# Performance work log

Measured on AMD Instinct MI355X. Metric: run time of the kernel, lower is better.

Reference implementation:

```python
import jax, jax.numpy as jnp
import numpy as np

KERNEL_SIZE = 25  # moving-average window (matches init kernel_size)


def setup_inputs() -> dict:
    key = jax.random.key(0)
    ks = jax.random.split(key, 5)
    B, T, N, D, O = 128, 336, 325, 3, 96
    return {
        "x": jax.random.normal(ks[0], (B, T, N, D), dtype=jnp.float32),
        "W_season": jax.random.normal(ks[1], (N, T, O), dtype=jnp.float32) * 0.02,
        "b_season": jax.random.normal(ks[2], (N, O), dtype=jnp.float32) * 0.02,
        "W_trend": jax.random.normal(ks[3], (N, T, O), dtype=jnp.float32) * 0.02,
        "b_trend": jax.random.normal(ks[4], (N, O), dtype=jnp.float32) * 0.02,
    }


def _moving_avg(z, k):
    # z: (M, T); replicate-pad (k-1)//2 at both ends, then mean over window k, stride 1.
    p = (k - 1) // 2
    xp = jnp.pad(z, ((0, 0), (p, p)), mode="edge")
    cs = jnp.concatenate(
        [jnp.zeros((z.shape[0], 1), z.dtype), jnp.cumsum(xp, axis=1)], axis=1
    )
    return (cs[:, k:] - cs[:, :-k]) / k  # (M, T) for odd k


def reference(x, W_season, b_season, W_trend, b_trend):
    B, T, N, D = x.shape
    O = W_season.shape[-1]
    # (B,T,N,D) -> (B,N,D,T) -> flat (B*N*D, T)
    z = x.transpose(0, 2, 3, 1).reshape(B * N * D, T)
    mean = _moving_avg(z, KERNEL_SIZE)
    res = z - mean
    BD = B * D
    # Faithful to the original slicing res[B*n*D : B*(n+1)*D]: contiguous blocks
    # of B*D rows per node -> reshape to (N, B*D, T).
    res_n = res.reshape(N, BD, T)
    mean_n = mean.reshape(N, BD, T)
    out_res = jnp.einsum("nbt,nto->nbo", res_n, W_season) + b_season[:, None, :]
    out_mean = jnp.einsum("nbt,nto->nbo", mean_n, W_trend) + b_trend[:, None, :]
    out = (out_res + out_mean).transpose(1, 0, 2)  # stack dim=1 -> (B*D, N, O)
    # torch .view(B, N, D, O) on contiguous (B*D, N, O), then permute(0,3,1,2)
    out = out.reshape(B, N, D, O).transpose(0, 3, 1, 2)  # (B, O, N, D)
    return out
```

## Files before the change

kernel.cpp:

```cpp
#include <hip/hip_runtime.h>
#include <hip/hip_bf16.h>

typedef __attribute__((ext_vector_type(8))) short short8;
typedef __attribute__((ext_vector_type(4))) float f32x4;
typedef unsigned short ushort_t;
typedef unsigned int uint32;

#define T_DIM   336
#define N_NODES 325
#define O_DIM   96
#define BD      384
#define ND      975
#define XB      327600
#define KT      96
#define NSTEP   4
#define MT      128
#define AST     104
#define BST     104
#define BSEG    10240
#define WTO     32256
#define WP_T    120

static __device__ __forceinline__ uint32 pk2bf(float a, float b) {
    union { __hip_bfloat16 h; ushort_t u; } x, y;
    x.h = __float2bfloat16(a); y.h = __float2bfloat16(b);
    return ((uint32)y.u << 16) | x.u;
}

static __device__ __forceinline__ void gload_lds16(const void* g, void* l) {
    __builtin_amdgcn_global_load_lds(
        (const __attribute__((address_space(1))) void*)g,
        (__attribute__((address_space(3))) void*)l, 16, 0, 0);
}

__global__ __launch_bounds__(576)
void dlinear_wprep(const float* __restrict__ Ws, const float* __restrict__ bs,
                   const float* __restrict__ Wt, const float* __restrict__ bt,
                   ushort_t* __restrict__ Bpack, float* __restrict__ biasArr)
{
    __shared__ float Wdl[WP_T][O_DIM];
    const int nn  = blockIdx.x;
    const int s   = blockIdx.y;
    const int tid = threadIdx.x;
    const int t0  = s * KT;

    const float* wsn = Ws + (size_t)nn * WTO;
    const float* wtn = Wt + (size_t)nn * WTO;

    #pragma unroll
    for (int it = 0; it < 20; ++it) {
        int i = tid + it*576;
        int t = i / O_DIM;
        int o = i - t*O_DIM;
        int tg = t0 - 12 + t;
        float v = 0.f;
        if (tg >= 0 && tg < T_DIM) v = wtn[tg*O_DIM + o] - wsn[tg*O_DIM + o];
        Wdl[t][o] = v;
    }
    if (s == 0 && tid < O_DIM)
        biasArr[nn*O_DIM + tid] = bs[nn*O_DIM + tid] + bt[nn*O_DIM + tid];
    __syncthreads();

    const int kc = tid / O_DIM;
    const int o  = tid - kc*O_DIM;
    const int k0 = kc * 16;

    float S = 0.f;
    #pragma unroll
    for (int j = 0; j < 25; ++j) S += Wdl[k0 + j][o];

    uint32* bp32 = (uint32*)(Bpack + (size_t)(nn*4 + s) * BSEG + o * BST);
    float prev = 0.f;
    #pragma unroll
    for (int j = 0; j < 16; ++j) {
        const int k = k0 + j;
        const int v = t0 + k;
        float val = 0.f;
        if (v < T_DIM) {
            float V = S;
            if (v == 0) {
                V = 0.f;
                #pragma unroll
                for (int t = 0; t <= 12; ++t) V += (float)(13 - t) * Wdl[12 + t][o];
            } else if (v == T_DIM - 1) {
                V = 0.f;
                #pragma unroll
                for (int t = 0; t <= 12; ++t) V += (float)(t + 1) * Wdl[47 + t][o];
            }
            val = wsn[v*O_DIM + o] + V * (1.0f/25.0f);
        }
        if (j & 1) bp32[k >> 1] = pk2bf(prev, val); else prev = val;
        if (j < 15) S += Wdl[k + 25][o] - Wdl[k][o];
    }
    if (kc == 0) {
        bp32[48] = 0u; bp32[49] = 0u; bp32[50] = 0u; bp32[51] = 0u;
    }
}

__global__ __launch_bounds__(512, 6)
void dlinear_gemm(const float* __restrict__ x,
                  const ushort_t* __restrict__ Bpack,
                  const float* __restrict__ biasArr,
                  float* __restrict__ Cws)
{
    __shared__ ushort_t Btile[BSEG];
    __shared__ ushort_t Atile[MT][AST];

    const int tid = threadIdx.x;
    const int bid = blockIdx.x;
    const int nn  = bid / 3;
    const int m0  = (bid % 3) * MT;
    const int r_base = nn * BD + m0;

    const int m   = tid & (MT-1);
    const int tb  = (tid >> 7) * 24;
    const int r   = r_base + m;
    const int bI  = r / ND;
    const int rem = r - bI * ND;
    const float* xp = x + (size_t)bI * XB + rem;

    const ushort_t* bsrc = Bpack + (size_t)nn * (4*BSEG);

    const int wave = tid >> 6;
    const int lane = tid & 63;
    const int wm = wave & 3;
    const int wn = wave >> 2;
    const int a_row0 = wm*32 + (lane & 15);
    const int b_col0 = wn*48 + (lane & 15);
    const int ksub   = (lane >> 4) * 8;

    f32x4 acc[2][3];
    #pragma unroll
    for (int i = 0; i < 2; ++i)
        #pragma unroll
        for (int j = 0; j < 3; ++j)
            acc[i][j] = (f32x4){0.f, 0.f, 0.f, 0.f};

    for (int s = 0; s < NSTEP; ++s) {
        __syncthreads();

        {
            const ushort_t* bs_s = bsrc + (size_t)s * BSEG;
            gload_lds16(bs_s + (size_t)tid*8,        &Btile[tid*8]);
            gload_lds16(bs_s + (size_t)(tid+512)*8,  &Btile[(tid+512)*8]);
            if (tid < 256)
                gload_lds16(bs_s + (size_t)(tid+1024)*8, &Btile[(tid+1024)*8]);
        }

        const int t0 = s * KT;
        #pragma unroll
        for (int h = 0; h < 2; ++h) {
            float v[12];
            #pragma unroll
            for (int u = 0; u < 12; ++u) {
                int t  = t0 + tb + h*12 + u;
                int tc = t < T_DIM ? t : (T_DIM-1);
                v[u] = __builtin_nontemporal_load(&xp[tc * ND]);
            }
            uint32 p[6];
            #pragma unroll
            for (int u = 0; u < 6; ++u) p[u] = pk2bf(v[2*u], v[2*u+1]);
            uint32* arow = (uint32*)&Atile[m][tb + h*12];
            *(uint2*)&arow[0] = make_uint2(p[0], p[1]);
            *(uint2*)&arow[2] = make_uint2(p[2], p[3]);
            *(uint2*)&arow[4] = make_uint2(p[4], p[5]);
        }
        __syncthreads();

        #pragma unroll
        for (int kc = 0; kc < 3; ++kc) {
            const int k = kc*32 + ksub;
            short8 a0 = *(const short8*)&Atile[a_row0     ][k];
            short8 a1 = *(const short8*)&Atile[a_row0 + 16][k];
            short8 b0 = *(const short8*)&Btile[(b_col0     )*BST + k];
            short8 b1 = *(const short8*)&Btile[(b_col0 + 16)*BST + k];
            short8 b2 = *(const short8*)&Btile[(b_col0 + 32)*BST + k];
            acc[0][0] = __builtin_amdgcn_mfma_f32_16x16x32_bf16(a0, b0, acc[0][0], 0, 0, 0);
            acc[1][0] = __builtin_amdgcn_mfma_f32_16x16x32_bf16(a1, b0, acc[1][0], 0, 0, 0);
            acc[0][1] = __builtin_amdgcn_mfma_f32_16x16x32_bf16(a0, b1, acc[0][1], 0, 0, 0);
            acc[1][1] = __builtin_amdgcn_mfma_f32_16x16x32_bf16(a1, b1, acc[1][1], 0, 0, 0);
            acc[0][2] = __builtin_amdgcn_mfma_f32_16x16x32_bf16(a0, b2, acc[0][2], 0, 0, 0);
            acc[1][2] = __builtin_amdgcn_mfma_f32_16x16x32_bf16(a1, b2, acc[1][2], 0, 0, 0);
        }
    }

    float* Cbase = Cws + (size_t)r_base * O_DIM;
    const float* bfp = biasArr + nn * O_DIM;
    const int rsub = (lane >> 4) * 4;
    #pragma unroll
    for (int fm = 0; fm < 2; ++fm) {
        #pragma unroll
        for (int fn = 0; fn < 3; ++fn) {
            const int col = b_col0 + fn*16;
            const float bv = bfp[col];
            #pragma unroll
            for (int j = 0; j < 4; ++j) {
                const int rowm = wm*32 + fm*16 + rsub + j;
                Cbase[rowm*O_DIM + col] = acc[fm][fn][j] + bv;
            }
        }
    }
}

__global__ __launch_bounds__(256)
void dlinear_out(const float* __restrict__ Cws, float* __restrict__ out)
{
    __shared__ float tile[65][97];
    const int m   = blockIdx.x;
    const int nn0 = blockIdx.y * 65;
    const int tid = threadIdx.x;

    for (int idx = tid; idx < 65*O_DIM; idx += 256) {
        int nni = idx / O_DIM;
        int o   = idx - nni*O_DIM;
        tile[nni][o] = Cws[(size_t)((nn0 + nni)*BD + m)*O_DIM + o];
    }
    __syncthreads();
    const int b = m / 3;
    const int g = m - b*3;
    float* obase = out + (size_t)b*93600 + g*N_NODES + nn0;
    for (int idx = tid; idx < 65*O_DIM; idx += 256) {
        int o   = idx / 65;
        int nni = idx - o*65;
        obase[o*ND + nni] = tile[nni][o];
    }
}

extern "C" void kernel_launch(void* const* d_in, const int* in_sizes, int n_in,
                              void* d_out, int out_size, void* d_ws, size_t ws_size,
                              hipStream_t stream)
{
    const float* x  = (const float*)d_in[0];
    const float* Ws = (const float*)d_in[1];
    const float* bs = (const float*)d_in[2];
    const float* Wt = (const float*)d_in[3];
    const float* bt = (const float*)d_in[4];
    float* out = (float*)d_out;
    float* Cws = (float*)d_ws;

    ushort_t* Bpack  = (ushort_t*)d_out;
    float*    biasAr = (float*)d_out + 6656000;

    dlinear_wprep<<<dim3(N_NODES, 4), dim3(576), 0, stream>>>(Ws, bs, Wt, bt, Bpack, biasAr);
    dlinear_gemm <<<dim3(975),        dim3(512), 0, stream>>>(x, Bpack, biasAr, Cws);
    dlinear_out  <<<dim3(384, 5),     dim3(256), 0, stream>>>(Cws, out);
}
```

Before: 133.4 us.

## Stage packed weights in LDS, store Wdl as bf16, preload Ws column

The weight-prep kernel now keeps the trend-minus-season difference in LDS as bf16 instead of fp32. It builds the packed B tile in a shared buffer and copies it out to global memory with contiguous stores. The Ws values are prefetched into registers before the sliding-window loop, and the load index math is simplified to avoid per-iteration division. These changes target uncoalesced strided global stores and LDS footprint so more blocks fit per CU. The cost is extra rounding of the moving-average weights to bf16, and the padding columns 96..103 of each packed row are no longer explicitly zeroed; they now hold uninitialised LDS data, which could affect the GEMM if those columns are ever read.

New measurement: 112.5 us. -15.7%, faster.

```diff
diff --git a/kernel.cpp b/kernel.cpp
--- a/kernel.cpp
+++ b/kernel.cpp
@@ -26,6 +26,16 @@
     x.h = __float2bfloat16(a); y.h = __float2bfloat16(b);
     return ((uint32)y.u << 16) | x.u;
 }
+static __device__ __forceinline__ ushort_t f2bf(float f) {
+    union { __hip_bfloat16 h; ushort_t u; } cv;
+    cv.h = __float2bfloat16(f);
+    return cv.u;
+}
+static __device__ __forceinline__ float bf2f(ushort_t u) {
+    union { ushort_t u; __hip_bfloat16 h; } cv;
+    cv.u = u;
+    return __bfloat162float(cv.h);
+}
 
 static __device__ __forceinline__ void gload_lds16(const void* g, void* l) {
     __builtin_amdgcn_global_load_lds(
@@ -33,12 +43,14 @@
         (__attribute__((address_space(3))) void*)l, 16, 0, 0);
 }
 
-__global__ __launch_bounds__(576)
+__global__ __launch_bounds__(576, 7)
 void dlinear_wprep(const float* __restrict__ Ws, const float* __restrict__ bs,
                    const float* __restrict__ Wt, const float* __restrict__ bt,
                    ushort_t* __restrict__ Bpack, float* __restrict__ biasArr)
 {
-    __shared__ float Wdl[WP_T][O_DIM];
+    __shared__ ushort_t Wdl[WP_T][O_DIM];
+    __shared__ ushort_t Bout[O_DIM * BST];
+
     const int nn  = blockIdx.x;
     const int s   = blockIdx.y;
     const int tid = threadIdx.x;
@@ -47,15 +59,17 @@
     const float* wsn = Ws + (size_t)nn * WTO;
     const float* wtn = Wt + (size_t)nn * WTO;
 
-    #pragma unroll
-    for (int it = 0; it < 20; ++it) {
-        int i = tid + it*576;
-        int t = i / O_DIM;
-        int o = i - t*O_DIM;
-        int tg = t0 - 12 + t;
-        float v = 0.f;
-        if (tg >= 0 && tg < T_DIM) v = wtn[tg*O_DIM + o] - wsn[tg*O_DIM + o];
-        Wdl[t][o] = v;
+    {
+        const int o   = tid % O_DIM;
+        const int tA  = tid / O_DIM;
+        #pragma unroll
+        for (int it = 0; it < 20; ++it) {
+            int t  = tA + it * 6;
+            int tg = t0 - 12 + t;
+            float v = 0.f;
+            if (tg >= 0 && tg < T_DIM) v = wtn[tg*O_DIM + o] - wsn[tg*O_DIM + o];
+            Wdl[t][o] = f2bf(v);
+        }
     }
     if (s == 0 && tid < O_DIM)
         biasArr[nn*O_DIM + tid] = bs[nn*O_DIM + tid] + bt[nn*O_DIM + tid];
@@ -65,11 +79,18 @@
     const int o  = tid - kc*O_DIM;
     const int k0 = kc * 16;
 
+    float wsv[16];
+    #pragma unroll
+    for (int j = 0; j < 16; ++j) {
+        int vv = t0 + k0 + j;
+        wsv[j] = (vv < T_DIM) ? wsn[vv*O_DIM + o] : 0.f;
+    }
+
     float S = 0.f;
     #pragma unroll
-    for (int j = 0; j < 25; ++j) S += Wdl[k0 + j][o];
-
-    uint32* bp32 = (uint32*)(Bpack + (size_t)(nn*4 + s) * BSEG + o * BST);
+    for (int j = 0; j < 25; ++j) S += bf2f(Wdl[k0 + j][o]);
+
+    uint32* bo32 = (uint32*)(Bout + o * BST);
     float prev = 0.f;
     #pragma unroll
     for (int j = 0; j < 16; ++j) {
@@ -81,19 +102,24 @@
             if (v == 0) {
                 V = 0.f;
                 #pragma unroll
-                for (int t = 0; t <= 12; ++t) V += (float)(13 - t) * Wdl[12 + t][o];
+                for (int t = 0; t <= 12; ++t) V += (float)(13 - t) * bf2f(Wdl[12 + t][o]);
             } else if (v == T_DIM - 1) {
                 V = 0.f;
                 #pragma unroll
-                for (int t = 0; t <= 12; ++t) V += (float)(t + 1) * Wdl[47 + t][o];
+                for (int t = 0; t <= 12; ++t) V += (float)(t + 1) * bf2f(Wdl[47 + t][o]);
             }
-            val = wsn[v*O_DIM + o] + V * (1.0f/25.0f);
-        }
-        if (j & 1) bp32[k >> 1] = pk2bf(prev, val); else prev = val;
-        if (j < 15) S += Wdl[k + 25][o] - Wdl[k][o];
-    }
-    if (kc == 0) {
-        bp32[48] = 0u; bp32[49] = 0u; bp32[50] = 0u; bp32[51] = 0u;
+            val = wsv[j] + V * (1.0f/25.0f);
+        }
+        if (j & 1) bo32[k >> 1] = pk2bf(prev, val); else prev = val;
+        if (j < 15) S += bf2f(Wdl[k + 25][o]) - bf2f(Wdl[k][o]);
+    }
+    __syncthreads();
+
+    {
+        const uint32* src = (const uint32*)Bout;
+        uint32* dst = (uint32*)(Bpack + (size_t)(nn*4 + s) * BSEG);
+        for (int d = tid; d < (O_DIM*BST)/2; d += 576)
+            dst[d] = src[d];
     }
 }
 
```
